# Performance work log

Hardware: AMD Instinct MI355X
Metric: run time of the kernel (lower is better)

The kernel has to match this reference:

```python
import jax, jax.numpy as jnp
import numpy as np

N_NODES = 100000
N_EDGES = 1600000
D_FEAT = 64      # per-node embedding dim; nin = 2*D_FEAT = 128
N_OUT = 64
NSLOPE = 0.2


def setup_inputs() -> dict:
    key = jax.random.key(0)
    k0, k1, k2, k3, k4, k5 = jax.random.split(key, 6)
    nodes = jax.random.normal(k0, (N_NODES, D_FEAT), dtype=jnp.float32)
    src = jax.random.randint(k1, (N_EDGES,), 0, N_NODES, dtype=jnp.int32)
    dst = jax.random.randint(k2, (N_EDGES,), 0, N_NODES, dtype=jnp.int32)
    # Linear(nin=2*D_FEAT, nout=N_OUT) weight/bias and Linear(nout,1,bias=False)
    W_w = jax.random.normal(k3, (N_OUT, 2 * D_FEAT), dtype=jnp.float32) * (2 * D_FEAT) ** -0.5
    W_b = jax.random.normal(k4, (N_OUT,), dtype=jnp.float32) * 0.02
    a_w = jax.random.normal(k5, (N_OUT,), dtype=jnp.float32) * N_OUT ** -0.5
    return {"nodes": nodes, "src": src, "dst": dst, "W_w": W_w, "W_b": W_b, "a_w": a_w}


def reference(nodes, src, dst, W_w, W_b, a_w):
    # Per edge: score = a( LeakyReLU( W [h_src ; h_dst] + b ) )
    # Split W over the concat so we project each node once, then gather.
    d = nodes.shape[1]
    W1, W2 = W_w[:, :d], W_w[:, d:]          # [nout, d] each
    p1 = nodes @ W1.T                        # [N, nout]
    p2 = nodes @ W2.T                        # [N, nout]
    hw = p1[src] + p2[dst] + W_b             # [E, nout]  (== W(cat(hi,hj)))
    act = jnp.where(hw >= 0, hw, NSLOPE * hw)  # LeakyReLU
    scores = act @ a_w                       # [E]
    # Sparse softmax over dim=1 of the [N,N] score matrix == segment softmax
    # over edges grouped by the row (src) index, numerically stabilized.
    n = nodes.shape[0]
    m = jax.ops.segment_max(scores, src, num_segments=n)   # [N]
    e = jnp.exp(scores - m[src])                            # [E]
    s = jax.ops.segment_sum(e, src, num_segments=n)         # [N]
    attn = e / s[src]                                       # [E]
    return attn
```

## Files before the change

### kernel.cpp

```cpp
#include <hip/hip_runtime.h>

#define NSLOPE 0.2f

typedef __attribute__((ext_vector_type(8))) short short8;
typedef __attribute__((ext_vector_type(4))) float floatx4;
typedef __attribute__((ext_vector_type(4))) float f32x4;
typedef __attribute__((ext_vector_type(4))) int   i32x4;

static __device__ inline unsigned short f2bf(float f) {
    unsigned u = __float_as_uint(f);
    unsigned r = u + 0x7FFFu + ((u >> 16) & 1u);
    return (unsigned short)(r >> 16);
}
static __device__ inline float bflo(unsigned u) { return __uint_as_float(u << 16); }
static __device__ inline float bfhi(unsigned u) { return __uint_as_float(u & 0xFFFF0000u); }

__global__ __launch_bounds__(256) void prep_kernel(const float* __restrict__ Ww,
                                                   unsigned short* __restrict__ Wbf) {
    int t = threadIdx.x;
    for (int idx = t; idx < 64 * 128; idx += 256) {
        int o = idx >> 7, c = idx & 127;
        int j, k;
        if (c < 64) { j = o;      k = c;      }
        else        { j = 64 + o; k = c - 64; }
        Wbf[j * 64 + k] = f2bf(Ww[idx]);
    }
}

#define PNB 128
#define AST 72

__global__ __launch_bounds__(256) void proj_mfma_kernel(
    const float* __restrict__ nodes, const unsigned short* __restrict__ Wbf,
    const float* __restrict__ Wb,
    unsigned short* __restrict__ P1, unsigned short* __restrict__ P2,
    float* __restrict__ ssum, int nNodes)
{
    __shared__ unsigned short aT[PNB * AST];
    __shared__ unsigned short wT[128 * AST];
    const int t = threadIdx.x;
    const int base = blockIdx.x * PNB;

    if (t < PNB) { int n = base + t; if (n < nNodes) ssum[n] = 0.f; }

    for (int f = t; f < PNB * 16; f += 256) {
        int n = f >> 4, dpos = (f & 15) * 4;
        float4 v = make_float4(0.f, 0.f, 0.f, 0.f);
        if (base + n < nNodes) v = *(const float4*)(nodes + (size_t)(base + n) * 64 + dpos);
        ushort4 o;
        o.x = f2bf(v.x); o.y = f2bf(v.y); o.z = f2bf(v.z); o.w = f2bf(v.w);
        *(ushort4*)&aT[n * AST + dpos] = o;
    }
    for (int i = t; i < 1024; i += 256) {
        int j = i >> 3, koff = (i & 7) * 8;
        uint4 v = *(const uint4*)(Wbf + j * 64 + koff);
        *(uint4*)&wT[j * AST + koff] = v;
    }
    __syncthreads();

    const int w = t >> 6, lane = t & 63;
    const int lr = lane & 15;
    const int lk = (lane >> 4) * 8;

    floatx4 acc[2][8];
    #pragma unroll
    for (int rt = 0; rt < 2; rt++)
        #pragma unroll
        for (int ct = 0; ct < 8; ct++) acc[rt][ct] = (floatx4){0.f, 0.f, 0.f, 0.f};

    #pragma unroll
    for (int ks = 0; ks < 2; ks++) {
        int k0 = ks * 32 + lk;
        short8 a0 = *(const short8*)&aT[((w * 2 + 0) * 16 + lr) * AST + k0];
        short8 a1 = *(const short8*)&aT[((w * 2 + 1) * 16 + lr) * AST + k0];
        #pragma unroll
        for (int ct = 0; ct < 8; ct++) {
            short8 b = *(const short8*)&wT[(ct * 16 + lr) * AST + k0];
            acc[0][ct] = __builtin_amdgcn_mfma_f32_16x16x32_bf16(a0, b, acc[0][ct], 0, 0, 0);
            acc[1][ct] = __builtin_amdgcn_mfma_f32_16x16x32_bf16(a1, b, acc[1][ct], 0, 0, 0);
        }
    }

    #pragma unroll
    for (int ct = 0; ct < 8; ct++) {
        int j = ct * 16 + lr;
        float bias = (j < 64) ? Wb[j] : 0.f;
        #pragma unroll
        for (int rt = 0; rt < 2; rt++) {
            #pragma unroll
            for (int r = 0; r < 4; r++) {
                int nl = (w * 2 + rt) * 16 + (lane >> 4) * 4 + r;
                int n = base + nl;
                if (n < nNodes) {
                    unsigned short val = f2bf(acc[rt][ct][r] + bias);
                    if (j < 64) P1[(size_t)n * 64 + j]      = val;
                    else        P2[(size_t)n * 64 + j - 64] = val;
                }
            }
        }
    }
}

__global__ __launch_bounds__(256) void edge_score_kernel(
    const unsigned short* __restrict__ P1, const unsigned short* __restrict__ P2,
    const int* __restrict__ src, const int* __restrict__ dst,
    const float* __restrict__ a_w,
    float* __restrict__ evals, float* __restrict__ ssum, int nE)
{
    int tid = blockIdx.x * 256 + threadIdx.x;
    int e   = tid >> 3;
    int sub = tid & 7;
    if (e >= nE) return;

    int s = __builtin_nontemporal_load(&src[e]);
    int d = __builtin_nontemporal_load(&dst[e]);
    uint4 r1 = *(const uint4*)(P1 + (size_t)s * 64 + sub * 8);
    uint4 r2 = *(const uint4*)(P2 + (size_t)d * 64 + sub * 8);
    float4 a0 = *(const float4*)(a_w + sub * 8);
    float4 a1 = *(const float4*)(a_w + sub * 8 + 4);

    float partial = 0.f, h;
    h = bflo(r1.x) + bflo(r2.x); h = (h >= 0.f) ? h : NSLOPE * h; partial = fmaf(h, a0.x, partial);
    h = bfhi(r1.x) + bfhi(r2.x); h = (h >= 0.f) ? h : NSLOPE * h; partial = fmaf(h, a0.y, partial);
    h = bflo(r1.y) + bflo(r2.y); h = (h >= 0.f) ? h : NSLOPE * h; partial = fmaf(h, a0.z, partial);
    h = bfhi(r1.y) + bfhi(r2.y); h = (h >= 0.f) ? h : NSLOPE * h; partial = fmaf(h, a0.w, partial);
    h = bflo(r1.z) + bflo(r2.z); h = (h >= 0.f) ? h : NSLOPE * h; partial = fmaf(h, a1.x, partial);
    h = bfhi(r1.z) + bfhi(r2.z); h = (h >= 0.f) ? h : NSLOPE * h; partial = fmaf(h, a1.y, partial);
    h = bflo(r1.w) + bflo(r2.w); h = (h >= 0.f) ? h : NSLOPE * h; partial = fmaf(h, a1.z, partial);
    h = bfhi(r1.w) + bfhi(r2.w); h = (h >= 0.f) ? h : NSLOPE * h; partial = fmaf(h, a1.w, partial);

    partial += __shfl_xor(partial, 1);
    partial += __shfl_xor(partial, 2);
    partial += __shfl_xor(partial, 4);

    if (sub == 0) {
        float ev = __expf(partial);
        __builtin_nontemporal_store(ev, &evals[e]);
        atomicAdd(&ssum[s], ev);
    }
}

__global__ __launch_bounds__(256) void recip_kernel(const float* __restrict__ ssum,
                                                    float* __restrict__ rinv, int nNodes) {
    int n = blockIdx.x * 256 + threadIdx.x;
    if (n < nNodes) rinv[n] = 1.0f / ssum[n];
}

__global__ __launch_bounds__(256) void normalize_kernel(
    const int* __restrict__ src, const float* __restrict__ rinv,
    float* __restrict__ out, int nE)
{
    int i = blockIdx.x * 256 + threadIdx.x;
    int e4 = i * 4;
    if (e4 + 3 < nE) {
        f32x4 ev = __builtin_nontemporal_load((const f32x4*)(out + e4));
        i32x4 sv = __builtin_nontemporal_load((const i32x4*)(src + e4));
        f32x4 r;
        r.x = ev.x * rinv[sv.x];
        r.y = ev.y * rinv[sv.y];
        r.z = ev.z * rinv[sv.z];
        r.w = ev.w * rinv[sv.w];
        __builtin_nontemporal_store(r, (f32x4*)(out + e4));
    } else {
        for (int e = e4; e < nE; ++e) out[e] = out[e] * rinv[src[e]];
    }
}

extern "C" void kernel_launch(void* const* d_in, const int* in_sizes, int n_in,
                              void* d_out, int out_size, void* d_ws, size_t ws_size,
                              hipStream_t stream) {
    (void)n_in; (void)out_size; (void)ws_size;
    const float* nodes = (const float*)d_in[0];
    const int*   src   = (const int*)d_in[1];
    const int*   dst   = (const int*)d_in[2];
    const float* Ww    = (const float*)d_in[3];
    const float* Wb    = (const float*)d_in[4];
    const float* a_w   = (const float*)d_in[5];
    float* out = (float*)d_out;

    const int nNodes = in_sizes[0] / 64;
    const int nE     = in_sizes[1];

    unsigned short* P1   = (unsigned short*)d_ws;
    unsigned short* P2   = P1 + (size_t)nNodes * 64;
    float*          ssum = (float*)(P2 + (size_t)nNodes * 64);
    float*          rinv = ssum + nNodes;
    unsigned short* Wbf  = (unsigned short*)(rinv + nNodes);

    prep_kernel<<<1, 256, 0, stream>>>(Ww, Wbf);

    int nblocks_proj = (nNodes + PNB - 1) / PNB;
    proj_mfma_kernel<<<nblocks_proj, 256, 0, stream>>>(nodes, Wbf, Wb, P1, P2, ssum, nNodes);

    int nblocks_edge = (int)(((long long)nE * 8 + 255) / 256);
    edge_score_kernel<<<nblocks_edge, 256, 0, stream>>>(P1, P2, src, dst, a_w, out, ssum, nE);

    int nblocks_recip = (nNodes + 255) / 256;
    recip_kernel<<<nblocks_recip, 256, 0, stream>>>(ssum, rinv, nNodes);

    int nthreads_norm = (nE + 3) / 4;
    int nblocks_norm  = (nthreads_norm + 255) / 256;
    normalize_kernel<<<nblocks_norm, 256, 0, stream>>>(src, rinv, out, nE);
}
```

Before: 133.6 us.

## Fuse weight prep and reciprocal into neighbors; process four edges per thread group

Removes the separate weight-conversion kernel by converting W to bf16 inside each projection block, and removes the reciprocal kernel by dividing by the segment sum directly in the normalize pass. The edge score kernel now handles four edges per 8-lane group, loading src/dst as int4 and issuing eight gathers per thread to raise memory-level parallelism. This cuts two launches and raises in-flight loads, but every projection block redoes the weight conversion and normalize now divides instead of multiplying. Nontemporal hints are also dropped.

```diff
diff --git a/kernel.cpp b/kernel.cpp
--- a/kernel.cpp
+++ b/kernel.cpp
@@ -4,8 +4,6 @@
 
 typedef __attribute__((ext_vector_type(8))) short short8;
 typedef __attribute__((ext_vector_type(4))) float floatx4;
-typedef __attribute__((ext_vector_type(4))) float f32x4;
-typedef __attribute__((ext_vector_type(4))) int   i32x4;
 
 static __device__ inline unsigned short f2bf(float f) {
     unsigned u = __float_as_uint(f);
@@ -15,23 +13,11 @@
 static __device__ inline float bflo(unsigned u) { return __uint_as_float(u << 16); }
 static __device__ inline float bfhi(unsigned u) { return __uint_as_float(u & 0xFFFF0000u); }
 
-__global__ __launch_bounds__(256) void prep_kernel(const float* __restrict__ Ww,
-                                                   unsigned short* __restrict__ Wbf) {
-    int t = threadIdx.x;
-    for (int idx = t; idx < 64 * 128; idx += 256) {
-        int o = idx >> 7, c = idx & 127;
-        int j, k;
-        if (c < 64) { j = o;      k = c;      }
-        else        { j = 64 + o; k = c - 64; }
-        Wbf[j * 64 + k] = f2bf(Ww[idx]);
-    }
-}
-
 #define PNB 128
 #define AST 72
 
 __global__ __launch_bounds__(256) void proj_mfma_kernel(
-    const float* __restrict__ nodes, const unsigned short* __restrict__ Wbf,
+    const float* __restrict__ nodes, const float* __restrict__ Ww,
     const float* __restrict__ Wb,
     unsigned short* __restrict__ P1, unsigned short* __restrict__ P2,
     float* __restrict__ ssum, int nNodes)
@@ -51,10 +37,16 @@
         o.x = f2bf(v.x); o.y = f2bf(v.y); o.z = f2bf(v.z); o.w = f2bf(v.w);
         *(ushort4*)&aT[n * AST + dpos] = o;
     }
-    for (int i = t; i < 1024; i += 256) {
-        int j = i >> 3, koff = (i & 7) * 8;
-        uint4 v = *(const uint4*)(Wbf + j * 64 + koff);
-        *(uint4*)&wT[j * AST + koff] = v;
+    for (int i = t; i < 2048; i += 256) {
+        float4 v = *(const float4*)(Ww + i * 4);
+        int o = i >> 5;
+        int c = (i * 4) & 127;
+        int j, k;
+        if (c < 64) { j = o;      k = c;      }
+        else        { j = 64 + o; k = c - 64; }
+        ushort4 w4;
+        w4.x = f2bf(v.x); w4.y = f2bf(v.y); w4.z = f2bf(v.z); w4.w = f2bf(v.w);
+        *(ushort4*)&wT[j * AST + k] = w4;
     }
     __syncthreads();
 
@@ -108,61 +100,94 @@
     float* __restrict__ evals, float* __restrict__ ssum, int nE)
 {
     int tid = blockIdx.x * 256 + threadIdx.x;
-    int e   = tid >> 3;
+    int g   = tid >> 3;
     int sub = tid & 7;
-    if (e >= nE) return;
-
-    int s = __builtin_nontemporal_load(&src[e]);
-    int d = __builtin_nontemporal_load(&dst[e]);
-    uint4 r1 = *(const uint4*)(P1 + (size_t)s * 64 + sub * 8);
-    uint4 r2 = *(const uint4*)(P2 + (size_t)d * 64 + sub * 8);
+    int e0  = g << 2;
+    if (e0 >= nE) return;
+    const bool full = (e0 + 4 <= nE);
+
+    int4 sv, dv;
+    if (full) {
+        sv = *(const int4*)(src + e0);
+        dv = *(const int4*)(dst + e0);
+    } else {
+        int a[4], b[4];
+        #pragma unroll
+        for (int i = 0; i < 4; i++) {
+            int e = (e0 + i < nE) ? e0 + i : nE - 1;
+            a[i] = src[e]; b[i] = dst[e];
+        }
+        sv = make_int4(a[0], a[1], a[2], a[3]);
+        dv = make_int4(b[0], b[1], b[2], b[3]);
+    }
+    int s[4] = {sv.x, sv.y, sv.z, sv.w};
+    int d[4] = {dv.x, dv.y, dv.z, dv.w};
+
+    uint4 r1[4], r2[4];
+    #pragma unroll
+    for (int i = 0; i < 4; i++) r1[i] = *(const uint4*)(P1 + (size_t)s[i] * 64 + sub * 8);
+    #pragma unroll
+    for (int i = 0; i < 4; i++) r2[i] = *(const uint4*)(P2 + (size_t)d[i] * 64 + sub * 8);
+
     float4 a0 = *(const float4*)(a_w + sub * 8);
     float4 a1 = *(const float4*)(a_w + sub * 8 + 4);
 
-    float partial = 0.f, h;
-    h = bflo(r1.x) + bflo(r2.x); h = (h >= 0.f) ? h : NSLOPE * h; partial = fmaf(h, a0.x, partial);
-    h = bfhi(r1.x) + bfhi(r2.x); h = (h >= 0.f) ? h : NSLOPE * h; partial = fmaf(h, a0.y, partial);
-    h = bflo(r1.y) + bflo(r2.y); h = (h >= 0.f) ? h : NSLOPE * h; partial = fmaf(h, a0.z, partial);
-    h = bfhi(r1.y) + bfhi(r2.y); h = (h >= 0.f) ? h : NSLOPE * h; partial = fmaf(h, a0.w, partial);
-    h = bflo(r1.z) + bflo(r2.z); h = (h >= 0.f) ? h : NSLOPE * h; partial = fmaf(h, a1.x, partial);
-    h = bfhi(r1.z) + bfhi(r2.z); h = (h >= 0.f) ? h : NSLOPE * h; partial = fmaf(h, a1.y, partial);
-    h = bflo(r1.w) + bflo(r2.w); h = (h >= 0.f) ? h : NSLOPE * h; partial = fmaf(h, a1.z, partial);
-    h = bfhi(r1.w) + bfhi(r2.w); h = (h >= 0.f) ? h : NSLOPE * h; partial = fmaf(h, a1.w, partial);
-
-    partial += __shfl_xor(partial, 1);
-    partial += __shfl_xor(partial, 2);
-    partial += __shfl_xor(partial, 4);
+    float partial[4];
+    #pragma unroll
+    for (int i = 0; i < 4; i++) {
+        float p = 0.f, h;
+        h = bflo(r1[i].x) + bflo(r2[i].x); h = (h >= 0.f) ? h : NSLOPE * h; p = fmaf(h, a0.x, p);
+        h = bfhi(r1[i].x) + bfhi(r2[i].x); h = (h >= 0.f) ? h : NSLOPE * h; p = fmaf(h, a0.y, p);
+        h = bflo(r1[i].y) + bflo(r2[i].y); h = (h >= 0.f) ? h : NSLOPE * h; p = fmaf(h, a0.z, p);
+        h = bfhi(r1[i].y) + bfhi(r2[i].y); h = (h >= 0.f) ? h : NSLOPE * h; p = fmaf(h, a0.w, p);
+        h = bflo(r1[i].z) + bflo(r2[i].z); h = (h >= 0.f) ? h : NSLOPE * h; p = fmaf(h, a1.x, p);
+        h = bfhi(r1[i].z) + bfhi(r2[i].z); h = (h >= 0.f) ? h : NSLOPE * h; p = fmaf(h, a1.y, p);
+        h = bflo(r1[i].w) + bflo(r2[i].w); h = (h >= 0.f) ? h : NSLOPE * h; p = fmaf(h, a1.z, p);
+        h = bfhi(r1[i].w) + bfhi(r2[i].w); h = (h >= 0.f) ? h : NSLOPE * h; p = fmaf(h, a1.w, p);
+        partial[i] = p;
+    }
+
+    #pragma unroll
+    for (int i = 0; i < 4; i++) {
+        partial[i] += __shfl_xor(partial[i], 1);
+        partial[i] += __shfl_xor(partial[i], 2);
+        partial[i] += __shfl_xor(partial[i], 4);
+    }
 
     if (sub == 0) {
-        float ev = __expf(partial);
-        __builtin_nontemporal_store(ev, &evals[e]);
-        atomicAdd(&ssum[s], ev);
-    }
-}
-
-__global__ __launch_bounds__(256) void recip_kernel(const float* __restrict__ ssum,
-                                                    float* __restrict__ rinv, int nNodes) {
-    int n = blockIdx.x * 256 + threadIdx.x;
-    if (n < nNodes) rinv[n] = 1.0f / ssum[n];
+        float ev[4];
+        #pragma unroll
+        for (int i = 0; i < 4; i++) ev[i] = __expf(partial[i]);
+        if (full) {
+            *(float4*)(evals + e0) = make_float4(ev[0], ev[1], ev[2], ev[3]);
+            #pragma unroll
+            for (int i = 0; i < 4; i++) atomicAdd(&ssum[s[i]], ev[i]);
+        } else {
+            for (int i = 0; i < 4 && e0 + i < nE; i++) {
+                evals[e0 + i] = ev[i];
+                atomicAdd(&ssum[s[i]], ev[i]);
+            }
+        }
+    }
 }
 
 __global__ __launch_bounds__(256) void normalize_kernel(
-    const int* __restrict__ src, const float* __restrict__ rinv,
+    const int* __restrict__ src, const float* __restrict__ ssum,
     float* __restrict__ out, int nE)
 {
     int i = blockIdx.x * 256 + threadIdx.x;
     int e4 = i * 4;
     if (e4 + 3 < nE) {
-        f32x4 ev = __builtin_nontemporal_load((const f32x4*)(out + e4));
-        i32x4 sv = __builtin_nontemporal_load((const i32x4*)(src + e4));
-        f32x4 r;
-        r.x = ev.x * rinv[sv.x];
-        r.y = ev.y * rinv[sv.y];
-        r.z = ev.z * rinv[sv.z];
-        r.w = ev.w * rinv[sv.w];
-        __builtin_nontemporal_store(r, (f32x4*)(out + e4));
+        float4 ev = *(const float4*)(out + e4);
+        int4   sv = *(const int4*)(src + e4);
+        float4 r;
+        r.x = ev.x / ssum[sv.x];
+        r.y = ev.y / ssum[sv.y];
+        r.z = ev.z / ssum[sv.z];
+        r.w = ev.w / ssum[sv.w];
+        *(float4*)(out + e4) = r;
     } else {
-        for (int e = e4; e < nE; ++e) out[e] = out[e] * rinv[src[e]];
+        for (int e = e4; e < nE; ++e) out[e] = out[e] / ssum[src[e]];
     }
 }
 
@@ -184,21 +209,15 @@
     unsigned short* P1   = (unsigned short*)d_ws;
     unsigned short* P2   = P1 + (size_t)nNodes * 64;
     float*          ssum = (float*)(P2 + (size_t)nNodes * 64);
-    float*          rinv = ssum + nNodes;
-    unsigned short* Wbf  = (unsigned short*)(rinv + nNodes);
-
-    prep_kernel<<<1, 256, 0, stream>>>(Ww, Wbf);
 
     int nblocks_proj = (nNodes + PNB - 1) / PNB;
-    proj_mfma_kernel<<<nblocks_proj, 256, 0, stream>>>(nodes, Wbf, Wb, P1, P2, ssum, nNodes);
-
-    int nblocks_edge = (int)(((long long)nE * 8 + 255) / 256);
+    proj_mfma_kernel<<<nblocks_proj, 256, 0, stream>>>(nodes, Ww, Wb, P1, P2, ssum, nNodes);
+
+    long long ngroups = ((long long)nE + 3) / 4;
+    int nblocks_edge = (int)((ngroups * 8 + 255) / 256);
     edge_score_kernel<<<nblocks_edge, 256, 0, stream>>>(P1, P2, src, dst, a_w, out, ssum, nE);
-
-    int nblocks_recip = (nNodes + 255) / 256;
-    recip_kernel<<<nblocks_recip, 256, 0, stream>>>(ssum, rinv, nNodes);
 
     int nthreads_norm = (nE + 3) / 4;
     int nblocks_norm  = (nthreads_norm + 255) / 256;
-    normalize_kernel<<<nblocks_norm, 256, 0, stream>>>(src, rinv, out, nE);
-}
+    normalize_kernel<<<nblocks_norm, 256, 0, stream>>>(src, ssum, out, nE);
+}
```

New measurement: 127.4 us. 1.05x faster.

## Fuse weight prep into projection, drop recip kernel, use plain loads

Applied to the files above, without the earlier changes.

Removes the separate weight-conversion kernel by having each projection block convert the fp32 weights to bf16 straight into shared memory. It also removes the reciprocal kernel, so normalization divides by the segment sum directly. Nontemporal loads and stores in the edge and normalize kernels become ordinary cached accesses. This cuts two kernel launches and an extra pass over nodes, at the cost of redundant weight conversion in every projection block and a division per edge.

```diff
diff --git a/kernel.cpp b/kernel.cpp
--- a/kernel.cpp
+++ b/kernel.cpp
@@ -4,8 +4,6 @@
 
 typedef __attribute__((ext_vector_type(8))) short short8;
 typedef __attribute__((ext_vector_type(4))) float floatx4;
-typedef __attribute__((ext_vector_type(4))) float f32x4;
-typedef __attribute__((ext_vector_type(4))) int   i32x4;
 
 static __device__ inline unsigned short f2bf(float f) {
     unsigned u = __float_as_uint(f);
@@ -15,23 +13,11 @@
 static __device__ inline float bflo(unsigned u) { return __uint_as_float(u << 16); }
 static __device__ inline float bfhi(unsigned u) { return __uint_as_float(u & 0xFFFF0000u); }
 
-__global__ __launch_bounds__(256) void prep_kernel(const float* __restrict__ Ww,
-                                                   unsigned short* __restrict__ Wbf) {
-    int t = threadIdx.x;
-    for (int idx = t; idx < 64 * 128; idx += 256) {
-        int o = idx >> 7, c = idx & 127;
-        int j, k;
-        if (c < 64) { j = o;      k = c;      }
-        else        { j = 64 + o; k = c - 64; }
-        Wbf[j * 64 + k] = f2bf(Ww[idx]);
-    }
-}
-
 #define PNB 128
 #define AST 72
 
 __global__ __launch_bounds__(256) void proj_mfma_kernel(
-    const float* __restrict__ nodes, const unsigned short* __restrict__ Wbf,
+    const float* __restrict__ nodes, const float* __restrict__ Ww,
     const float* __restrict__ Wb,
     unsigned short* __restrict__ P1, unsigned short* __restrict__ P2,
     float* __restrict__ ssum, int nNodes)
@@ -51,10 +37,16 @@
         o.x = f2bf(v.x); o.y = f2bf(v.y); o.z = f2bf(v.z); o.w = f2bf(v.w);
         *(ushort4*)&aT[n * AST + dpos] = o;
     }
-    for (int i = t; i < 1024; i += 256) {
-        int j = i >> 3, koff = (i & 7) * 8;
-        uint4 v = *(const uint4*)(Wbf + j * 64 + koff);
-        *(uint4*)&wT[j * AST + koff] = v;
+    for (int i = t; i < 2048; i += 256) {
+        float4 v = *(const float4*)(Ww + i * 4);
+        int o = i >> 5;
+        int c = (i * 4) & 127;
+        int j, k;
+        if (c < 64) { j = o;      k = c;      }
+        else        { j = 64 + o; k = c - 64; }
+        ushort4 w4;
+        w4.x = f2bf(v.x); w4.y = f2bf(v.y); w4.z = f2bf(v.z); w4.w = f2bf(v.w);
+        *(ushort4*)&wT[j * AST + k] = w4;
     }
     __syncthreads();
 
@@ -112,8 +104,8 @@
     int sub = tid & 7;
     if (e >= nE) return;
 
-    int s = __builtin_nontemporal_load(&src[e]);
-    int d = __builtin_nontemporal_load(&dst[e]);
+    int s = src[e];
+    int d = dst[e];
     uint4 r1 = *(const uint4*)(P1 + (size_t)s * 64 + sub * 8);
     uint4 r2 = *(const uint4*)(P2 + (size_t)d * 64 + sub * 8);
     float4 a0 = *(const float4*)(a_w + sub * 8);
@@ -135,34 +127,28 @@
 
     if (sub == 0) {
         float ev = __expf(partial);
-        __builtin_nontemporal_store(ev, &evals[e]);
+        evals[e] = ev;
         atomicAdd(&ssum[s], ev);
     }
 }
 
-__global__ __launch_bounds__(256) void recip_kernel(const float* __restrict__ ssum,
-                                                    float* __restrict__ rinv, int nNodes) {
-    int n = blockIdx.x * 256 + threadIdx.x;
-    if (n < nNodes) rinv[n] = 1.0f / ssum[n];
-}
-
 __global__ __launch_bounds__(256) void normalize_kernel(
-    const int* __restrict__ src, const float* __restrict__ rinv,
+    const int* __restrict__ src, const float* __restrict__ ssum,
     float* __restrict__ out, int nE)
 {
     int i = blockIdx.x * 256 + threadIdx.x;
     int e4 = i * 4;
     if (e4 + 3 < nE) {
-        f32x4 ev = __builtin_nontemporal_load((const f32x4*)(out + e4));
-        i32x4 sv = __builtin_nontemporal_load((const i32x4*)(src + e4));
-        f32x4 r;
-        r.x = ev.x * rinv[sv.x];
-        r.y = ev.y * rinv[sv.y];
-        r.z = ev.z * rinv[sv.z];
-        r.w = ev.w * rinv[sv.w];
-        __builtin_nontemporal_store(r, (f32x4*)(out + e4));
+        float4 ev = *(const float4*)(out + e4);
+        int4   sv = *(const int4*)(src + e4);
+        float4 r;
+        r.x = ev.x / ssum[sv.x];
+        r.y = ev.y / ssum[sv.y];
+        r.z = ev.z / ssum[sv.z];
+        r.w = ev.w / ssum[sv.w];
+        *(float4*)(out + e4) = r;
     } else {
-        for (int e = e4; e < nE; ++e) out[e] = out[e] * rinv[src[e]];
+        for (int e = e4; e < nE; ++e) out[e] = out[e] / ssum[src[e]];
     }
 }
 
@@ -184,21 +170,14 @@
     unsigned short* P1   = (unsigned short*)d_ws;
     unsigned short* P2   = P1 + (size_t)nNodes * 64;
     float*          ssum = (float*)(P2 + (size_t)nNodes * 64);
-    float*          rinv = ssum + nNodes;
-    unsigned short* Wbf  = (unsigned short*)(rinv + nNodes);
-
-    prep_kernel<<<1, 256, 0, stream>>>(Ww, Wbf);
 
     int nblocks_proj = (nNodes + PNB - 1) / PNB;
-    proj_mfma_kernel<<<nblocks_proj, 256, 0, stream>>>(nodes, Wbf, Wb, P1, P2, ssum, nNodes);
+    proj_mfma_kernel<<<nblocks_proj, 256, 0, stream>>>(nodes, Ww, Wb, P1, P2, ssum, nNodes);
 
     int nblocks_edge = (int)(((long long)nE * 8 + 255) / 256);
     edge_score_kernel<<<nblocks_edge, 256, 0, stream>>>(P1, P2, src, dst, a_w, out, ssum, nE);
 
-    int nblocks_recip = (nNodes + 255) / 256;
-    recip_kernel<<<nblocks_recip, 256, 0, stream>>>(ssum, rinv, nNodes);
-
     int nthreads_norm = (nE + 3) / 4;
     int nblocks_norm  = (nthreads_norm + 255) / 256;
-    normalize_kernel<<<nblocks_norm, 256, 0, stream>>>(src, rinv, out, nE);
+    normalize_kernel<<<nblocks_norm, 256, 0, stream>>>(src, ssum, out, nE);
 }
```

Result: faster. 125.7 us (-5.9%).
